# Performance work log

Hardware: AMD Instinct MI355X
Metric: run time of the kernel (lower is better)

Reference implementation:

```python
import jax, jax.numpy as jnp
import numpy as np

CUTOFF = 5.0
N_ATOMS, N_EDGES, D, R = 100000, 1600000, 64, 20


def setup_inputs() -> dict:
    key = jax.random.key(0)
    ks = jax.random.split(key, 12)
    ve = jax.random.normal(ks[0], (N_ATOMS, D, 3), dtype=jnp.float32)
    se = jax.random.normal(ks[1], (N_ATOMS, D), dtype=jnp.float32)
    dirs = jax.random.normal(ks[2], (N_EDGES, 3), dtype=jnp.float32)
    dirs = dirs / jnp.linalg.norm(dirs, axis=-1, keepdims=True)
    dist = jax.random.uniform(ks[3], (N_EDGES,), minval=0.5, maxval=CUTOFF, dtype=jnp.float32)
    nv = dirs * dist[:, None]  # neighbour_vectors with norm in (0.5, cutoff)
    central = jax.random.randint(ks[4], (N_EDGES,), 0, N_ATOMS)
    neigh = jax.random.randint(ks[5], (N_EDGES,), 0, N_ATOMS)
    # Bessel frequencies n*pi/cutoff (learnable in graph-pes)
    freqs = (jnp.arange(1, R + 1, dtype=jnp.float32) * np.pi / CUTOFF)
    W_filter = jax.random.normal(ks[6], (R, 3 * D), dtype=jnp.float32) / np.sqrt(R)
    b_filter = jnp.zeros((3 * D,), dtype=jnp.float32)
    W1 = jax.random.normal(ks[7], (D, D), dtype=jnp.float32) / np.sqrt(D)
    b1 = jnp.zeros((D,), dtype=jnp.float32)
    W2 = jax.random.normal(ks[8], (D, 3 * D), dtype=jnp.float32) / np.sqrt(D)
    b2 = jnp.zeros((3 * D,), dtype=jnp.float32)
    return {
        'vector_embeddings': ve, 'scalar_embeddings': se, 'neighbour_vectors': nv,
        'central_atoms': central, 'neighbours': neigh,
        'freqs': freqs, 'W_filter': W_filter, 'b_filter': b_filter,
        'W1': W1, 'b1': b1, 'W2': W2, 'b2': b2,
    }


def _envelope(d):
    # polynomial envelope, p = 6
    u = d / CUTOFF
    env = 1.0 - 28.0 * u**6 + 48.0 * u**7 - 21.0 * u**8
    return jnp.where(d < CUTOFF, env, 0.0)


def reference(vector_embeddings, scalar_embeddings, neighbour_vectors,
              central_atoms, neighbours, freqs, W_filter, b_filter,
              W1, b1, W2, b2):
    d = jnp.linalg.norm(neighbour_vectors, axis=-1)                 # [E]
    unit = neighbour_vectors / d[:, None]                           # [E, 3]
    # Bessel radial basis: sqrt(2/c) * sin(f_n d) / d
    bessel = np.sqrt(2.0 / CUTOFF) * jnp.sin(freqs[None, :] * d[:, None]) / d[:, None]  # [E, R]
    filt = (bessel @ W_filter + b_filter) * _envelope(d)[:, None]   # [E, 3D]
    # phi: MLP [D, D, 3D] with SiLU between layers
    h = jax.nn.silu(scalar_embeddings @ W1 + b1) @ W2 + b2          # [N, 3D]
    x_ij = filt * h[central_atoms]                                  # [E, 3D]
    a, b, c = jnp.split(x_ij, 3, axis=-1)                           # each [E, D]
    n = scalar_embeddings.shape[0]
    delta_s = jax.ops.segment_sum(a, neighbours, num_segments=n)    # [N, D]
    v_ij = b[:, :, None] * unit[:, None, :] + c[:, :, None] * vector_embeddings[neighbours]  # [E, D, 3]
    delta_v = jax.ops.segment_sum(v_ij, neighbours, num_segments=n)  # [N, D, 3]
    return (delta_v, delta_s)
```

## Files before the change

### kernel.cpp

```cpp
#include <hip/hip_runtime.h>
#include <math.h>

#define DCH 64
#define TD 192
#define RR 20
#define FCUT 5.0f

typedef __attribute__((ext_vector_type(8))) short short8;
typedef __attribute__((ext_vector_type(4))) float f32x4;

__device__ __forceinline__ unsigned short f2bf(float f) {
    unsigned int u = __float_as_uint(f);
    u += 0x7FFFu + ((u >> 16) & 1u);
    return (unsigned short)(u >> 16);
}

__global__ __launch_bounds__(256, 2) void mlp_mfma_kernel(
    const float* __restrict__ se,
    const float* __restrict__ W1, const float* __restrict__ b1,
    const float* __restrict__ W2, const float* __restrict__ b2,
    float* __restrict__ h, int N)
{
    const int wid  = threadIdx.x >> 6;
    const int lane = threadIdx.x & 63;
    const int g    = lane >> 4;
    const int c    = lane & 15;

    __shared__ float hmid[4][16][68];

    short8 W1f[4][2];
    float  b1t[4];
    #pragma unroll
    for (int t = 0; t < 4; ++t) {
        #pragma unroll
        for (int kh = 0; kh < 2; ++kh)
            #pragma unroll
            for (int j = 0; j < 8; ++j) {
                int k = kh * 32 + 8 * g + j;
                W1f[t][kh][j] = (short)f2bf(W1[k * DCH + 16 * t + c]);
            }
        b1t[t] = b1[16 * t + c];
    }
    short8 W2f[12][2];
    float  b2t[12];
    #pragma unroll
    for (int t = 0; t < 12; ++t) {
        #pragma unroll
        for (int kh = 0; kh < 2; ++kh)
            #pragma unroll
            for (int j = 0; j < 8; ++j) {
                int k = kh * 32 + 8 * g + j;
                W2f[t][kh][j] = (short)f2bf(W2[k * TD + 16 * t + c]);
            }
        b2t[t] = b2[16 * t + c];
    }

    for (int base = blockIdx.x * 64; base < N; base += gridDim.x * 64) {
        const int arow = base + wid * 16;
        const int atom = arow + c;
        const bool va  = atom < N;

        const float* sp = se + (size_t)(va ? atom : 0) * DCH;
        short8 A0, A1;
        #pragma unroll
        for (int kh = 0; kh < 2; ++kh) {
            float4 q0 = va ? *(const float4*)(sp + kh*32 + 8*g)     : make_float4(0,0,0,0);
            float4 q1 = va ? *(const float4*)(sp + kh*32 + 8*g + 4) : make_float4(0,0,0,0);
            short8& A = kh ? A1 : A0;
            A[0] = (short)f2bf(q0.x); A[1] = (short)f2bf(q0.y);
            A[2] = (short)f2bf(q0.z); A[3] = (short)f2bf(q0.w);
            A[4] = (short)f2bf(q1.x); A[5] = (short)f2bf(q1.y);
            A[6] = (short)f2bf(q1.z); A[7] = (short)f2bf(q1.w);
        }

        #pragma unroll
        for (int t = 0; t < 4; ++t) {
            f32x4 C = {0.f, 0.f, 0.f, 0.f};
            C = __builtin_amdgcn_mfma_f32_16x16x32_bf16(A0, W1f[t][0], C, 0, 0, 0);
            C = __builtin_amdgcn_mfma_f32_16x16x32_bf16(A1, W1f[t][1], C, 0, 0, 0);
            #pragma unroll
            for (int reg = 0; reg < 4; ++reg) {
                float x = C[reg] + b1t[t];
                float s = x / (1.0f + __expf(-x));
                hmid[wid][4 * g + reg][16 * t + c] = s;
            }
        }
        __syncthreads();

        short8 B0, B1;
        #pragma unroll
        for (int kh = 0; kh < 2; ++kh) {
            const float* hp = &hmid[wid][c][kh * 32 + 8 * g];
            float4 q0 = *(const float4*)(hp);
            float4 q1 = *(const float4*)(hp + 4);
            short8& A = kh ? B1 : B0;
            A[0] = (short)f2bf(q0.x); A[1] = (short)f2bf(q0.y);
            A[2] = (short)f2bf(q0.z); A[3] = (short)f2bf(q0.w);
            A[4] = (short)f2bf(q1.x); A[5] = (short)f2bf(q1.y);
            A[6] = (short)f2bf(q1.z); A[7] = (short)f2bf(q1.w);
        }

        #pragma unroll
        for (int t = 0; t < 12; ++t) {
            f32x4 C = {0.f, 0.f, 0.f, 0.f};
            C = __builtin_amdgcn_mfma_f32_16x16x32_bf16(B0, W2f[t][0], C, 0, 0, 0);
            C = __builtin_amdgcn_mfma_f32_16x16x32_bf16(B1, W2f[t][1], C, 0, 0, 0);
            #pragma unroll
            for (int reg = 0; reg < 4; ++reg) {
                int a2 = arow + 4 * g + reg;
                if (a2 < N)
                    h[(size_t)a2 * TD + 16 * t + c] = C[reg] + b2t[t];
            }
        }
        __syncthreads();
    }
}

__global__ void hist_kernel(const int* __restrict__ neigh,
                            int* __restrict__ counts, int* __restrict__ pos, int E)
{
    int stride = gridDim.x * blockDim.x;
    for (int e = blockIdx.x * blockDim.x + threadIdx.x; e < E; e += stride)
        pos[e] = atomicAdd(&counts[neigh[e]], 1);
}

__global__ __launch_bounds__(256) void scan1_kernel(
    const int* __restrict__ counts, int* __restrict__ starts,
    int* __restrict__ bsums, int N)
{
    int tid = threadIdx.x;
    int gid = blockIdx.x * 256 + tid;
    int v = (gid < N) ? counts[gid] : 0;
    int lane = tid & 63, wid = tid >> 6;
    int x = v;
    #pragma unroll
    for (int off = 1; off < 64; off <<= 1) {
        int y = __shfl_up(x, off, 64);
        if (lane >= off) x += y;
    }
    __shared__ int wsum[4];
    if (lane == 63) wsum[wid] = x;
    __syncthreads();
    int add = 0;
    for (int w = 0; w < wid; ++w) add += wsum[w];
    int incl = x + add;
    if (gid < N) starts[gid] = incl - v;
    if (tid == 255) bsums[blockIdx.x] = incl;
}

__global__ __launch_bounds__(512) void scan2_kernel(int* __restrict__ bsums, int M)
{
    int tid = threadIdx.x;
    int v = (tid < M) ? bsums[tid] : 0;
    int lane = tid & 63, wid = tid >> 6;
    int x = v;
    #pragma unroll
    for (int off = 1; off < 64; off <<= 1) {
        int y = __shfl_up(x, off, 64);
        if (lane >= off) x += y;
    }
    __shared__ int wsum[8];
    if (lane == 63) wsum[wid] = x;
    __syncthreads();
    int add = 0;
    for (int w = 0; w < wid; ++w) add += wsum[w];
    int incl = x + add;
    if (tid < M) bsums[tid] = incl - v;
}

__global__ __launch_bounds__(256) void scan3_kernel(
    int* __restrict__ starts, const int* __restrict__ bsums, int N)
{
    int gid = blockIdx.x * 256 + threadIdx.x;
    if (gid < N) starts[gid] += bsums[blockIdx.x];
}

__global__ void fill_kernel(const float* __restrict__ nv, const int* __restrict__ central,
                            const int* __restrict__ neigh, const int* __restrict__ starts,
                            const int* __restrict__ pos, float4* __restrict__ payload, int E)
{
    int stride = gridDim.x * blockDim.x;
    for (int e = blockIdx.x * blockDim.x + threadIdx.x; e < E; e += stride) {
        int slot = starts[neigh[e]] + pos[e];
        payload[slot] = make_float4(nv[(size_t)e*3+0], nv[(size_t)e*3+1],
                                    nv[(size_t)e*3+2], __int_as_float(central[e]));
    }
}

__global__ __launch_bounds__(256) void gather_kernel(
    const float4* __restrict__ payload, const int* __restrict__ starts,
    const int* __restrict__ counts, const float* __restrict__ h,
    const float* __restrict__ ve, const float* __restrict__ Wf,
    const float* __restrict__ bfil,
    float* __restrict__ dv, float* __restrict__ ds, int N)
{
    const int wid  = threadIdx.x >> 6;
    const int lane = threadIdx.x & 63;
    const int g    = lane >> 4;
    const int c    = lane & 15;

    short8 Bf[12];
    float  bft[12];
    #pragma unroll
    for (int t = 0; t < 12; ++t) {
        #pragma unroll
        for (int j = 0; j < 8; ++j) {
            int r = 8 * g + j;
            float w = (r < RR) ? Wf[r * TD + 16 * t + c] : 0.0f;
            Bf[t][j] = (short)f2bf(w);
        }
        bft[t] = bfil[16 * t + c];
    }

    const float BC = sqrtf(2.0f / FCUT);
    const float XK = (float)(M_PI / (double)FCUT);
    const char* hb = (const char*)h;

    for (int atom = blockIdx.x * 4 + wid; atom < N; atom += gridDim.x * 4) {
        const int s   = starts[atom];
        const int cnt = counts[atom];

        float dsa[4] = {0,0,0,0};
        float csm[4] = {0,0,0,0};
        float dvx[4] = {0,0,0,0};
        float dvy[4] = {0,0,0,0};
        float dvz[4] = {0,0,0,0};

        for (int i0 = 0; i0 < cnt; i0 += 16) {
            const bool valid = (i0 + c) < cnt;
            float4 p = valid ? payload[s + i0 + c]
                             : make_float4(1.0f, 0.0f, 0.0f, __int_as_float(0));
            float dist = sqrtf(p.x*p.x + p.y*p.y + p.z*p.z);
            float inv  = 1.0f / dist;
            float xa   = dist * XK;

            float u  = dist * (1.0f / FCUT);
            float u2 = u * u;
            float u6 = u2 * u2 * u2;
            float env = 1.0f + u6 * (-28.0f + u * (48.0f - 21.0f * u));
            env = (dist < FCUT && valid) ? env : 0.0f;
            float scale = BC * inv * env;

            float ux = p.x * inv, uy = p.y * inv, uz = p.z * inv;
            int   hof = __float_as_int(p.w) * (TD * 4);

            float bas[8];
            bas[0] = __sinf((float)(8 * g + 1) * xa);
            bas[1] = __sinf((float)(8 * g + 2) * xa);
            float twoc = 2.0f * __cosf(xa);
            #pragma unroll
            for (int j = 2; j < 8; ++j)
                bas[j] = fmaf(twoc, bas[j-1], -bas[j-2]);

            short8 A;
            #pragma unroll
            for (int j = 0; j < 8; ++j)
                A[j] = (short)f2bf(bas[j] * scale);

            float env_r[4], ux_r[4], uy_r[4], uz_r[4];
            int   hof_r[4];
            #pragma unroll
            for (int reg = 0; reg < 4; ++reg) {
                int src = 4 * g + reg;
                env_r[reg] = __shfl(env, src, 64);
                ux_r[reg]  = __shfl(ux,  src, 64);
                uy_r[reg]  = __shfl(uy,  src, 64);
                uz_r[reg]  = __shfl(uz,  src, 64);
                hof_r[reg] = __shfl(hof, src, 64);
            }
            const float* hp[4];
            #pragma unroll
            for (int reg = 0; reg < 4; ++reg)
                hp[reg] = (const float*)(hb + (size_t)(unsigned)hof_r[reg]) + c;

            #pragma unroll
            for (int t = 0; t < 4; ++t) {
                f32x4 C = __builtin_amdgcn_mfma_f32_16x16x32_bf16(
                    A, Bf[t], (f32x4){0.f,0.f,0.f,0.f}, 0, 0, 0);
                #pragma unroll
                for (int reg = 0; reg < 4; ++reg) {
                    float hv = hp[reg][16 * t];
                    float filt = fmaf(bft[t], env_r[reg], C[reg]);
                    dsa[t] = fmaf(filt, hv, dsa[t]);
                }
            }
            #pragma unroll
            for (int t = 4; t < 8; ++t) {
                f32x4 C = __builtin_amdgcn_mfma_f32_16x16x32_bf16(
                    A, Bf[t], (f32x4){0.f,0.f,0.f,0.f}, 0, 0, 0);
                #pragma unroll
                for (int reg = 0; reg < 4; ++reg) {
                    float hv = hp[reg][16 * t];
                    float filt = fmaf(bft[t], env_r[reg], C[reg]);
                    float bh = filt * hv;
                    dvx[t-4] = fmaf(bh, ux_r[reg], dvx[t-4]);
                    dvy[t-4] = fmaf(bh, uy_r[reg], dvy[t-4]);
                    dvz[t-4] = fmaf(bh, uz_r[reg], dvz[t-4]);
                }
            }
            #pragma unroll
            for (int t = 8; t < 12; ++t) {
                f32x4 C = __builtin_amdgcn_mfma_f32_16x16x32_bf16(
                    A, Bf[t], (f32x4){0.f,0.f,0.f,0.f}, 0, 0, 0);
                #pragma unroll
                for (int reg = 0; reg < 4; ++reg) {
                    float hv = hp[reg][16 * t];
                    float filt = fmaf(bft[t], env_r[reg], C[reg]);
                    csm[t-8] = fmaf(filt, hv, csm[t-8]);
                }
            }
        }

        #pragma unroll
        for (int t = 0; t < 4; ++t) {
            dsa[t] += __shfl_xor(dsa[t], 16, 64); dsa[t] += __shfl_xor(dsa[t], 32, 64);
            csm[t] += __shfl_xor(csm[t], 16, 64); csm[t] += __shfl_xor(csm[t], 32, 64);
            dvx[t] += __shfl_xor(dvx[t], 16, 64); dvx[t] += __shfl_xor(dvx[t], 32, 64);
            dvy[t] += __shfl_xor(dvy[t], 16, 64); dvy[t] += __shfl_xor(dvy[t], 32, 64);
            dvz[t] += __shfl_xor(dvz[t], 16, 64); dvz[t] += __shfl_xor(dvz[t], 32, 64);
        }

        float dssel = (g==0) ? dsa[0] : (g==1) ? dsa[1] : (g==2) ? dsa[2] : dsa[3];
        float cssel = (g==0) ? csm[0] : (g==1) ? csm[1] : (g==2) ? csm[2] : csm[3];
        float vxsel = (g==0) ? dvx[0] : (g==1) ? dvx[1] : (g==2) ? dvx[2] : dvx[3];
        float vysel = (g==0) ? dvy[0] : (g==1) ? dvy[1] : (g==2) ? dvy[2] : dvy[3];
        float vzsel = (g==0) ? dvz[0] : (g==1) ? dvz[1] : (g==2) ? dvz[2] : dvz[3];

        int ch = 16 * g + c;
        size_t vb = (size_t)atom * TD + (size_t)ch * 3;
        float v0 = ve[vb + 0], v1 = ve[vb + 1], v2 = ve[vb + 2];
        dv[vb + 0] = fmaf(cssel, v0, vxsel);
        dv[vb + 1] = fmaf(cssel, v1, vysel);
        dv[vb + 2] = fmaf(cssel, v2, vzsel);
        ds[(size_t)atom * DCH + ch] = dssel;
    }
}

extern "C" void kernel_launch(void* const* d_in, const int* in_sizes, int n_in,
                              void* d_out, int out_size, void* d_ws, size_t ws_size,
                              hipStream_t stream) {
    const float* ve      = (const float*)d_in[0];
    const float* se      = (const float*)d_in[1];
    const float* nv      = (const float*)d_in[2];
    const int*   central = (const int*)  d_in[3];
    const int*   neigh   = (const int*)  d_in[4];
    const float* Wf      = (const float*)d_in[6];
    const float* bfil    = (const float*)d_in[7];
    const float* W1      = (const float*)d_in[8];
    const float* b1      = (const float*)d_in[9];
    const float* W2      = (const float*)d_in[10];
    const float* b2      = (const float*)d_in[11];

    const int N = in_sizes[1] / DCH;
    const int E = in_sizes[3];

    float* out = (float*)d_out;
    float* dv  = out;
    float* ds  = out + (size_t)N * TD;

    char* wsb = (char*)d_ws;
    size_t off = 0;
    auto wsalloc = [&](size_t bytes) -> void* {
        void* p = wsb + off;
        off = (off + bytes + 255) & ~(size_t)255;
        return p;
    };
    float*  h       = (float*) wsalloc((size_t)N * TD * 4);
    int*    counts  = (int*)   wsalloc((size_t)N * 4);
    int*    starts  = (int*)   wsalloc((size_t)N * 4);
    int*    pos     = (int*)   wsalloc((size_t)E * 4);
    float4* payload = (float4*)wsalloc((size_t)E * 16);
    int*    bsums   = (int*)   wsalloc(4096);

    const int nb1 = (N + 255) / 256;
    const int nbm = (N + 63) / 64;

    mlp_mfma_kernel<<<nbm, 256, 0, stream>>>(se, W1, b1, W2, b2, h, N);

    hipMemsetAsync(counts, 0, (size_t)N * 4, stream);
    hist_kernel<<<2048, 256, 0, stream>>>(neigh, counts, pos, E);
    scan1_kernel<<<nb1, 256, 0, stream>>>(counts, starts, bsums, N);
    scan2_kernel<<<1, 512, 0, stream>>>(bsums, nb1);
    scan3_kernel<<<nb1, 256, 0, stream>>>(starts, bsums, N);
    fill_kernel<<<2048, 256, 0, stream>>>(nv, central, neigh, starts, pos, payload, E);
    gather_kernel<<<2048, 256, 0, stream>>>(payload, starts, counts, h, ve,
                                            Wf, bfil, dv, ds, N);
}
```

Baseline: 390.9 us.

## Store MLP output h as bf16 in a channel-interleaved layout and add nontemporal hints

Result: faster. 354.0 us (-9.5%).

```diff
diff --git a/kernel.cpp b/kernel.cpp
--- a/kernel.cpp
+++ b/kernel.cpp
@@ -8,18 +8,25 @@
 
 typedef __attribute__((ext_vector_type(8))) short short8;
 typedef __attribute__((ext_vector_type(4))) float f32x4;
+typedef __attribute__((ext_vector_type(2))) unsigned int u32x2;
 
 __device__ __forceinline__ unsigned short f2bf(float f) {
     unsigned int u = __float_as_uint(f);
     u += 0x7FFFu + ((u >> 16) & 1u);
     return (unsigned short)(u >> 16);
 }
+__device__ __forceinline__ float bflo(unsigned int u) {
+    return __uint_as_float(u << 16);
+}
+__device__ __forceinline__ float bfhi(unsigned int u) {
+    return __uint_as_float(u & 0xFFFF0000u);
+}
 
 __global__ __launch_bounds__(256, 2) void mlp_mfma_kernel(
     const float* __restrict__ se,
     const float* __restrict__ W1, const float* __restrict__ b1,
     const float* __restrict__ W2, const float* __restrict__ b2,
-    float* __restrict__ h, int N)
+    unsigned short* __restrict__ h2, int N)
 {
     const int wid  = threadIdx.x >> 6;
     const int lane = threadIdx.x & 63;
@@ -27,6 +34,7 @@
     const int c    = lane & 15;
 
     __shared__ float hmid[4][16][68];
+    __shared__ unsigned short hstage[4][16][196];
 
     short8 W1f[4][2];
     float  b1t[4];
@@ -64,13 +72,15 @@
         short8 A0, A1;
         #pragma unroll
         for (int kh = 0; kh < 2; ++kh) {
-            float4 q0 = va ? *(const float4*)(sp + kh*32 + 8*g)     : make_float4(0,0,0,0);
-            float4 q1 = va ? *(const float4*)(sp + kh*32 + 8*g + 4) : make_float4(0,0,0,0);
+            f32x4 q0 = va ? __builtin_nontemporal_load((const f32x4*)(sp + kh*32 + 8*g))
+                          : (f32x4){0.f,0.f,0.f,0.f};
+            f32x4 q1 = va ? __builtin_nontemporal_load((const f32x4*)(sp + kh*32 + 8*g + 4))
+                          : (f32x4){0.f,0.f,0.f,0.f};
             short8& A = kh ? A1 : A0;
-            A[0] = (short)f2bf(q0.x); A[1] = (short)f2bf(q0.y);
-            A[2] = (short)f2bf(q0.z); A[3] = (short)f2bf(q0.w);
-            A[4] = (short)f2bf(q1.x); A[5] = (short)f2bf(q1.y);
-            A[6] = (short)f2bf(q1.z); A[7] = (short)f2bf(q1.w);
+            A[0] = (short)f2bf(q0[0]); A[1] = (short)f2bf(q0[1]);
+            A[2] = (short)f2bf(q0[2]); A[3] = (short)f2bf(q0[3]);
+            A[4] = (short)f2bf(q1[0]); A[5] = (short)f2bf(q1[1]);
+            A[6] = (short)f2bf(q1[2]); A[7] = (short)f2bf(q1[3]);
         }
 
         #pragma unroll
@@ -91,13 +101,13 @@
         #pragma unroll
         for (int kh = 0; kh < 2; ++kh) {
             const float* hp = &hmid[wid][c][kh * 32 + 8 * g];
-            float4 q0 = *(const float4*)(hp);
-            float4 q1 = *(const float4*)(hp + 4);
+            f32x4 q0 = *(const f32x4*)(hp);
+            f32x4 q1 = *(const f32x4*)(hp + 4);
             short8& A = kh ? B1 : B0;
-            A[0] = (short)f2bf(q0.x); A[1] = (short)f2bf(q0.y);
-            A[2] = (short)f2bf(q0.z); A[3] = (short)f2bf(q0.w);
-            A[4] = (short)f2bf(q1.x); A[5] = (short)f2bf(q1.y);
-            A[6] = (short)f2bf(q1.z); A[7] = (short)f2bf(q1.w);
+            A[0] = (short)f2bf(q0[0]); A[1] = (short)f2bf(q0[1]);
+            A[2] = (short)f2bf(q0[2]); A[3] = (short)f2bf(q0[3]);
+            A[4] = (short)f2bf(q1[0]); A[5] = (short)f2bf(q1[1]);
+            A[6] = (short)f2bf(q1[2]); A[7] = (short)f2bf(q1[3]);
         }
 
         #pragma unroll
@@ -106,13 +116,20 @@
             C = __builtin_amdgcn_mfma_f32_16x16x32_bf16(B0, W2f[t][0], C, 0, 0, 0);
             C = __builtin_amdgcn_mfma_f32_16x16x32_bf16(B1, W2f[t][1], C, 0, 0, 0);
             #pragma unroll
-            for (int reg = 0; reg < 4; ++reg) {
-                int a2 = arow + 4 * g + reg;
+            for (int reg = 0; reg < 4; ++reg)
+                hstage[wid][4 * g + reg][c * 12 + t] = f2bf(C[reg] + b2t[t]);
+        }
+        __syncthreads();
+
+        if (lane < 48) {
+            #pragma unroll
+            for (int i = 0; i < 16; ++i) {
+                int a2 = arow + i;
                 if (a2 < N)
-                    h[(size_t)a2 * TD + 16 * t + c] = C[reg] + b2t[t];
-            }
-        }
-        __syncthreads();
+                    *(u32x2*)((char*)h2 + (size_t)a2 * 384 + lane * 8) =
+                        *(const u32x2*)(&hstage[wid][i][lane * 4]);
+            }
+        }
     }
 }
 
@@ -120,8 +137,10 @@
                             int* __restrict__ counts, int* __restrict__ pos, int E)
 {
     int stride = gridDim.x * blockDim.x;
-    for (int e = blockIdx.x * blockDim.x + threadIdx.x; e < E; e += stride)
-        pos[e] = atomicAdd(&counts[neigh[e]], 1);
+    for (int e = blockIdx.x * blockDim.x + threadIdx.x; e < E; e += stride) {
+        int p = atomicAdd(&counts[neigh[e]], 1);
+        __builtin_nontemporal_store(p, &pos[e]);
+    }
 }
 
 __global__ __launch_bounds__(256) void scan1_kernel(
@@ -177,19 +196,23 @@
 
 __global__ void fill_kernel(const float* __restrict__ nv, const int* __restrict__ central,
                             const int* __restrict__ neigh, const int* __restrict__ starts,
-                            const int* __restrict__ pos, float4* __restrict__ payload, int E)
+                            const int* __restrict__ pos, f32x4* __restrict__ payload, int E)
 {
     int stride = gridDim.x * blockDim.x;
     for (int e = blockIdx.x * blockDim.x + threadIdx.x; e < E; e += stride) {
         int slot = starts[neigh[e]] + pos[e];
-        payload[slot] = make_float4(nv[(size_t)e*3+0], nv[(size_t)e*3+1],
-                                    nv[(size_t)e*3+2], __int_as_float(central[e]));
+        f32x4 pay;
+        pay[0] = __builtin_nontemporal_load(&nv[(size_t)e*3+0]);
+        pay[1] = __builtin_nontemporal_load(&nv[(size_t)e*3+1]);
+        pay[2] = __builtin_nontemporal_load(&nv[(size_t)e*3+2]);
+        pay[3] = __int_as_float(central[e]);
+        __builtin_nontemporal_store(pay, &payload[slot]);
     }
 }
 
 __global__ __launch_bounds__(256) void gather_kernel(
-    const float4* __restrict__ payload, const int* __restrict__ starts,
-    const int* __restrict__ counts, const float* __restrict__ h,
+    const f32x4* __restrict__ payload, const int* __restrict__ starts,
+    const int* __restrict__ counts, const unsigned short* __restrict__ h2,
     const float* __restrict__ ve, const float* __restrict__ Wf,
     const float* __restrict__ bfil,
     float* __restrict__ dv, float* __restrict__ ds, int N)
@@ -214,7 +237,7 @@
 
     const float BC = sqrtf(2.0f / FCUT);
     const float XK = (float)(M_PI / (double)FCUT);
-    const char* hb = (const char*)h;
+    const char* hb = (const char*)h2;
 
     for (int atom = blockIdx.x * 4 + wid; atom < N; atom += gridDim.x * 4) {
         const int s   = starts[atom];
@@ -228,9 +251,9 @@
 
         for (int i0 = 0; i0 < cnt; i0 += 16) {
             const bool valid = (i0 + c) < cnt;
-            float4 p = valid ? payload[s + i0 + c]
-                             : make_float4(1.0f, 0.0f, 0.0f, __int_as_float(0));
-            float dist = sqrtf(p.x*p.x + p.y*p.y + p.z*p.z);
+            f32x4 p = valid ? __builtin_nontemporal_load(&payload[s + i0 + c])
+                            : (f32x4){1.0f, 0.0f, 0.0f, 0.0f};
+            float dist = sqrtf(p[0]*p[0] + p[1]*p[1] + p[2]*p[2]);
             float inv  = 1.0f / dist;
             float xa   = dist * XK;
 
@@ -241,8 +264,9 @@
             env = (dist < FCUT && valid) ? env : 0.0f;
             float scale = BC * inv * env;
 
-            float ux = p.x * inv, uy = p.y * inv, uz = p.z * inv;
-            int   hof = __float_as_int(p.w) * (TD * 4);
+            float ux = p[0] * inv, uy = p[1] * inv, uz = p[2] * inv;
+            int   ca  = valid ? __float_as_int(p[3]) : 0;
+            int   hof = ca * 384;
 
             float bas[8];
             bas[0] = __sinf((float)(8 * g + 1) * xa);
@@ -268,45 +292,35 @@
                 uz_r[reg]  = __shfl(uz,  src, 64);
                 hof_r[reg] = __shfl(hof, src, 64);
             }
-            const float* hp[4];
-            #pragma unroll
-            for (int reg = 0; reg < 4; ++reg)
-                hp[reg] = (const float*)(hb + (size_t)(unsigned)hof_r[reg]) + c;
-
-            #pragma unroll
-            for (int t = 0; t < 4; ++t) {
+
+            u32x2 hq[4][3];
+            #pragma unroll
+            for (int reg = 0; reg < 4; ++reg) {
+                const char* rp = hb + (size_t)(unsigned)hof_r[reg] + c * 24;
+                hq[reg][0] = *(const u32x2*)(rp);
+                hq[reg][1] = *(const u32x2*)(rp + 8);
+                hq[reg][2] = *(const u32x2*)(rp + 16);
+            }
+
+            #pragma unroll
+            for (int t = 0; t < 12; ++t) {
                 f32x4 C = __builtin_amdgcn_mfma_f32_16x16x32_bf16(
                     A, Bf[t], (f32x4){0.f,0.f,0.f,0.f}, 0, 0, 0);
                 #pragma unroll
                 for (int reg = 0; reg < 4; ++reg) {
-                    float hv = hp[reg][16 * t];
+                    unsigned int w = hq[reg][t >> 2][(t >> 1) & 1];
+                    float hv = (t & 1) ? bfhi(w) : bflo(w);
                     float filt = fmaf(bft[t], env_r[reg], C[reg]);
-                    dsa[t] = fmaf(filt, hv, dsa[t]);
-                }
-            }
-            #pragma unroll
-            for (int t = 4; t < 8; ++t) {
-                f32x4 C = __builtin_amdgcn_mfma_f32_16x16x32_bf16(
-                    A, Bf[t], (f32x4){0.f,0.f,0.f,0.f}, 0, 0, 0);
-                #pragma unroll
-                for (int reg = 0; reg < 4; ++reg) {
-                    float hv = hp[reg][16 * t];
-                    float filt = fmaf(bft[t], env_r[reg], C[reg]);
-                    float bh = filt * hv;
-                    dvx[t-4] = fmaf(bh, ux_r[reg], dvx[t-4]);
-                    dvy[t-4] = fmaf(bh, uy_r[reg], dvy[t-4]);
-                    dvz[t-4] = fmaf(bh, uz_r[reg], dvz[t-4]);
-                }
-            }
-            #pragma unroll
-            for (int t = 8; t < 12; ++t) {
-                f32x4 C = __builtin_amdgcn_mfma_f32_16x16x32_bf16(
-                    A, Bf[t], (f32x4){0.f,0.f,0.f,0.f}, 0, 0, 0);
-                #pragma unroll
-                for (int reg = 0; reg < 4; ++reg) {
-                    float hv = hp[reg][16 * t];
-                    float filt = fmaf(bft[t], env_r[reg], C[reg]);
-                    csm[t-8] = fmaf(filt, hv, csm[t-8]);
+                    if (t < 4) {
+                        dsa[t] = fmaf(filt, hv, dsa[t]);
+                    } else if (t < 8) {
+                        float bh = filt * hv;
+                        dvx[t-4] = fmaf(bh, ux_r[reg], dvx[t-4]);
+                        dvy[t-4] = fmaf(bh, uy_r[reg], dvy[t-4]);
+                        dvz[t-4] = fmaf(bh, uz_r[reg], dvz[t-4]);
+                    } else {
+                        csm[t-8] = fmaf(filt, hv, csm[t-8]);
+                    }
                 }
             }
         }
@@ -328,11 +342,13 @@
 
         int ch = 16 * g + c;
         size_t vb = (size_t)atom * TD + (size_t)ch * 3;
-        float v0 = ve[vb + 0], v1 = ve[vb + 1], v2 = ve[vb + 2];
-        dv[vb + 0] = fmaf(cssel, v0, vxsel);
-        dv[vb + 1] = fmaf(cssel, v1, vysel);
-        dv[vb + 2] = fmaf(cssel, v2, vzsel);
-        ds[(size_t)atom * DCH + ch] = dssel;
+        float v0 = __builtin_nontemporal_load(&ve[vb + 0]);
+        float v1 = __builtin_nontemporal_load(&ve[vb + 1]);
+        float v2 = __builtin_nontemporal_load(&ve[vb + 2]);
+        __builtin_nontemporal_store(fmaf(cssel, v0, vxsel), &dv[vb + 0]);
+        __builtin_nontemporal_store(fmaf(cssel, v1, vysel), &dv[vb + 1]);
+        __builtin_nontemporal_store(fmaf(cssel, v2, vzsel), &dv[vb + 2]);
+        __builtin_nontemporal_store(dssel, &ds[(size_t)atom * DCH + ch]);
     }
 }
 
@@ -365,17 +381,17 @@
         off = (off + bytes + 255) & ~(size_t)255;
         return p;
     };
-    float*  h       = (float*) wsalloc((size_t)N * TD * 4);
-    int*    counts  = (int*)   wsalloc((size_t)N * 4);
-    int*    starts  = (int*)   wsalloc((size_t)N * 4);
-    int*    pos     = (int*)   wsalloc((size_t)E * 4);
-    float4* payload = (float4*)wsalloc((size_t)E * 16);
-    int*    bsums   = (int*)   wsalloc(4096);
+    unsigned short* h2      = (unsigned short*)wsalloc((size_t)N * 192 * 2);
+    int*            counts  = (int*)   wsalloc((size_t)N * 4);
+    int*            starts  = (int*)   wsalloc((size_t)N * 4);
+    int*            pos     = (int*)   wsalloc((size_t)E * 4);
+    f32x4*          payload = (f32x4*) wsalloc((size_t)E * 16);
+    int*            bsums   = (int*)   wsalloc(4096);
 
     const int nb1 = (N + 255) / 256;
     const int nbm = (N + 63) / 64;
 
-    mlp_mfma_kernel<<<nbm, 256, 0, stream>>>(se, W1, b1, W2, b2, h, N);
+    mlp_mfma_kernel<<<nbm, 256, 0, stream>>>(se, W1, b1, W2, b2, h2, N);
 
     hipMemsetAsync(counts, 0, (size_t)N * 4, stream);
     hist_kernel<<<2048, 256, 0, stream>>>(neigh, counts, pos, E);
@@ -383,6 +399,6 @@
     scan2_kernel<<<1, 512, 0, stream>>>(bsums, nb1);
     scan3_kernel<<<nb1, 256, 0, stream>>>(starts, bsums, N);
     fill_kernel<<<2048, 256, 0, stream>>>(nv, central, neigh, starts, pos, payload, E);
-    gather_kernel<<<2048, 256, 0, stream>>>(payload, starts, counts, h, ve,
+    gather_kernel<<<2048, 256, 0, stream>>>(payload, starts, counts, h2, ve,
                                             Wf, bfil, dv, ds, N);
 }
```
